# Performance work log

Measured on AMD Instinct MI355X. Metric: run time of the kernel, lower is better.

## Reference

```python
import jax, jax.numpy as jnp
import numpy as np

B, L, D = 2, 2048, 1024
H, DH = 16, 64
HIDDEN = 4096
DILATION, WINDOW, CAUSAL = 2, 512, True
EPS = 1e-5


def _ln(x, g, b):
    m = jnp.mean(x, axis=-1, keepdims=True)
    v = jnp.mean(jnp.square(x - m), axis=-1, keepdims=True)
    return (x - m) * jax.lax.rsqrt(v + EPS) * g + b


def setup_inputs() -> dict:
    key = jax.random.key(0)
    ks = jax.random.split(key, 8)
    s = 0.02
    return {
        "x": jax.random.normal(ks[0], (B, L, D), jnp.float32),
        "ln1_g": jnp.ones((D,), jnp.float32),
        "ln1_b": jnp.zeros((D,), jnp.float32),
        "w_qkv": jax.random.normal(ks[1], (3 * D, D), jnp.float32) * s,
        "b_qkv": jnp.zeros((3 * D,), jnp.float32),
        "w_o": jax.random.normal(ks[2], (D, D), jnp.float32) * s,
        "b_o": jnp.zeros((D,), jnp.float32),
        "ln2_g": jnp.ones((D,), jnp.float32),
        "ln2_b": jnp.zeros((D,), jnp.float32),
        "w_ff1": jax.random.normal(ks[3], (HIDDEN, D), jnp.float32) * s,
        "b_ff1": jnp.zeros((HIDDEN,), jnp.float32),
        "w_ff2": jax.random.normal(ks[4], (D, HIDDEN), jnp.float32) * s,
        "b_ff2": jnp.zeros((D,), jnp.float32),
    }


def reference(x, ln1_g, ln1_b, w_qkv, b_qkv, w_o, b_o, ln2_g, ln2_b, w_ff1, b_ff1, w_ff2, b_ff2):
    # pre-norm attention block with dilated/windowed/causal mask
    h = _ln(x, ln1_g, ln1_b)
    qkv = h @ w_qkv.T + b_qkv                      # [B, L, 3D]
    q, k, v = jnp.split(qkv, 3, axis=-1)
    q = q.reshape(B, L, H, DH)
    k = k.reshape(B, L, H, DH)
    v = v.reshape(B, L, H, DH)

    scale = 1.0 / jnp.sqrt(jnp.float32(DH))
    scores = jnp.einsum("bqhd,bkhd->bhqk", q, k) * scale  # [B, H, L, L]

    i = jnp.arange(L)[:, None]
    j = jnp.arange(L)[None, :]
    allowed = ((i - j) % DILATION == 0) & (jnp.abs(i - j) <= WINDOW)
    if CAUSAL:
        allowed = allowed & (j <= i)
    scores = jnp.where(allowed, scores, -jnp.inf)  # diagonal always allowed -> rows finite

    p = jax.nn.softmax(scores, axis=-1)
    attn = jnp.einsum("bhqk,bkhd->bqhd", p, v).reshape(B, L, D)

    out = x + attn @ w_o.T + b_o                   # residual 1 (dropout p=0)

    h2 = _ln(out, ln2_g, ln2_b)
    ff = jax.nn.gelu(h2 @ w_ff1.T + b_ff1, approximate=False) @ w_ff2.T + b_ff2
    return out + ff                                # residual 2
```

## Files before the change

kernel.cpp:

```cpp
#include <hip/hip_runtime.h>
#include <hip/hip_bf16.h>
#include <cmath>

#define Bsz 2
#define Lseq 2048
#define Dmod 1024
#define Hhead 16
#define DH 64
#define HID 4096
#define ROWS (Bsz * Lseq)
#define TD (3 * Dmod)

typedef __attribute__((ext_vector_type(8))) short bf16x8;
typedef __attribute__((ext_vector_type(4))) float f32x4;
typedef unsigned short ushort_t;

typedef const __attribute__((address_space(1))) void gv_t;
typedef __attribute__((address_space(3))) void lv_t;
#define GLDS16(GP, LP) __builtin_amdgcn_global_load_lds((gv_t*)(GP), (lv_t*)(LP), 16, 0, 0)

__device__ __forceinline__ float bf2f(short u)
{
    return __uint_as_float(((unsigned)(unsigned short)u) << 16);
}
__device__ __forceinline__ unsigned pack2(float a, float b)
{
    __hip_bfloat162 t;
    t.x = __float2bfloat16(a);
    t.y = __float2bfloat16(b);
    return *reinterpret_cast<unsigned*>(&t);
}
__device__ __forceinline__ float gelu_exact(float t)
{
    return 0.5f * t * (1.0f + erff(t * 0.70710678118654752f));
}

__device__ __forceinline__ void xcd_remap2(int cn, int cm, int& mblk, int& nblk)
{
    int nx = gridDim.x;
    int id = blockIdx.y * nx + blockIdx.x;
    int xcd = id & 7;
    int local = id >> 3;
    int gxn = nx / cn;
    int gx = xcd % gxn, gy = xcd / gxn;
    int ln = local % cn, lm = local / cn;
    nblk = gx * cn + ln;
    mblk = gy * cm + lm;
}

__global__ __launch_bounds__(256) void conv_q_ln1(const float* __restrict__ wsrc, ushort_t* __restrict__ wdst,
                                                  const float* __restrict__ x,
                                                  const float* __restrict__ g,
                                                  const float* __restrict__ bta,
                                                  ushort_t* __restrict__ lnout)
{
    int blk = blockIdx.x;
    int t = threadIdx.x;
    if (blk < 3072) {
        int i = blk * 256 + t;
        float4 v = reinterpret_cast<const float4*>(wsrc)[i];
        uint2 o;
        o.x = pack2(v.x, v.y);
        o.y = pack2(v.z, v.w);
        reinterpret_cast<uint2*>(wdst)[i] = o;
        return;
    }
    int row = blk - 3072;
    const float4* xr = reinterpret_cast<const float4*>(x) + (size_t)row * 256;
    float4 v = xr[t];
    float sum1 = v.x + v.y + v.z + v.w;
    float sum2 = v.x * v.x + v.y * v.y + v.z * v.z + v.w * v.w;
#pragma unroll
    for (int o = 32; o > 0; o >>= 1) {
        sum1 += __shfl_down(sum1, o);
        sum2 += __shfl_down(sum2, o);
    }
    __shared__ float sa[4], sb[4];
    int wv = t >> 6, ln = t & 63;
    if (ln == 0) { sa[wv] = sum1; sb[wv] = sum2; }
    __syncthreads();
    sum1 = sa[0] + sa[1] + sa[2] + sa[3];
    sum2 = sb[0] + sb[1] + sb[2] + sb[3];
    float mean = sum1 * (1.0f / 1024.0f);
    float var  = sum2 * (1.0f / 1024.0f) - mean * mean;
    float inv  = rsqrtf(var + 1e-5f);
    float4 gv = reinterpret_cast<const float4*>(g)[t];
    float4 bv = reinterpret_cast<const float4*>(bta)[t];
    uint2 o;
    o.x = pack2((v.x - mean) * inv * gv.x + bv.x, (v.y - mean) * inv * gv.y + bv.y);
    o.y = pack2((v.z - mean) * inv * gv.z + bv.z, (v.w - mean) * inv * gv.w + bv.w);
    reinterpret_cast<uint2*>(lnout)[(size_t)row * 256 + t] = o;
}

__global__ __launch_bounds__(256) void ln_kernel(const float* __restrict__ x,
                                                 const float* __restrict__ g,
                                                 const float* __restrict__ bta,
                                                 ushort_t* __restrict__ out)
{
    int row = blockIdx.x;
    int t = threadIdx.x;
    const float4* xr = reinterpret_cast<const float4*>(x) + (size_t)row * 256;
    float4 v = xr[t];
    float sum1 = v.x + v.y + v.z + v.w;
    float sum2 = v.x * v.x + v.y * v.y + v.z * v.z + v.w * v.w;
#pragma unroll
    for (int o = 32; o > 0; o >>= 1) {
        sum1 += __shfl_down(sum1, o);
        sum2 += __shfl_down(sum2, o);
    }
    __shared__ float sa[4], sb[4];
    int wv = t >> 6, ln = t & 63;
    if (ln == 0) { sa[wv] = sum1; sb[wv] = sum2; }
    __syncthreads();
    sum1 = sa[0] + sa[1] + sa[2] + sa[3];
    sum2 = sb[0] + sb[1] + sb[2] + sb[3];
    float mean = sum1 * (1.0f / 1024.0f);
    float var  = sum2 * (1.0f / 1024.0f) - mean * mean;
    float inv  = rsqrtf(var + 1e-5f);
    float4 gv = reinterpret_cast<const float4*>(g)[t];
    float4 bv = reinterpret_cast<const float4*>(bta)[t];
    uint2 o;
    o.x = pack2((v.x - mean) * inv * gv.x + bv.x, (v.y - mean) * inv * gv.y + bv.y);
    o.y = pack2((v.z - mean) * inv * gv.z + bv.z, (v.w - mean) * inv * gv.w + bv.w);
    reinterpret_cast<uint2*>(out)[(size_t)row * 256 + t] = o;
}

__device__ __forceinline__ void gemm_n64_body(const ushort_t* __restrict__ A,
                                              const ushort_t* __restrict__ W,
                                              const float* __restrict__ bias,
                                              const float* __restrict__ res,
                                              void* __restrict__ C,
                                              int M, int N, int K, int ldw,
                                              int act, int obf, int cn, int cm)
{
    __shared__ ushort_t As0[128 * 64];
    __shared__ ushort_t Bs0[64 * 64];
    __shared__ ushort_t As1[128 * 64];
    __shared__ ushort_t Bs1[64 * 64];

    int tid = threadIdx.x;
    int w = tid >> 6, lane = tid & 63;
    int mblk, nblk;
    xcd_remap2(cn, cm, mblk, nblk);
    int m0 = mblk * 128, n0 = nblk * 64;
    int wr = (w >> 1) * 64, wc = (w & 1) * 32;

    int srow = lane >> 3;
    int scol = (((lane & 7) ^ (lane >> 3)) & 7) * 8;
    const ushort_t* ga[4];
    const ushort_t* gb[2];
    int laofs[4], lbofs[2];
#pragma unroll
    for (int q = 0; q < 4; ++q) {
        ga[q] = A + (size_t)(m0 + w * 32 + q * 8 + srow) * K + scol;
        laofs[q] = (w * 32 + q * 8) * 64;
    }
#pragma unroll
    for (int q = 0; q < 2; ++q) {
        gb[q] = W + (size_t)(n0 + w * 16 + q * 8 + srow) * ldw + scol;
        lbofs[q] = (w * 16 + q * 8) * 64;
    }

    int fr = lane & 15;
    int fg = lane >> 4;
    int r0 = fg * 4;
    int cc = fr;

    f32x4 acc[4][2] = {};

    auto stage = [&](ushort_t* AS, ushort_t* BS, int k0) {
#pragma unroll
        for (int q = 0; q < 4; ++q) GLDS16(ga[q] + k0, AS + laofs[q]);
#pragma unroll
        for (int q = 0; q < 2; ++q) GLDS16(gb[q] + k0, BS + lbofs[q]);
    };
    auto compute = [&](const ushort_t* AS, const ushort_t* BS) {
#pragma unroll
        for (int kk = 0; kk < 2; ++kk) {
            bf16x8 af[4], bfr[2];
            int ca = ((kk * 4 + fg) ^ (fr & 7)) * 8;
#pragma unroll
            for (int i = 0; i < 4; ++i)
                af[i] = *reinterpret_cast<const bf16x8*>(&AS[(wr + i * 16 + fr) * 64 + ca]);
#pragma unroll
            for (int i = 0; i < 2; ++i)
                bfr[i] = *reinterpret_cast<const bf16x8*>(&BS[(wc + i * 16 + fr) * 64 + ca]);
#pragma unroll
            for (int mi = 0; mi < 4; ++mi)
#pragma unroll
                for (int ni = 0; ni < 2; ++ni)
                    acc[mi][ni] = __builtin_amdgcn_mfma_f32_16x16x32_bf16(
                        af[mi], bfr[ni], acc[mi][ni], 0, 0, 0);
        }
    };

    int nt = K >> 6;
    stage(As0, Bs0, 0);
    stage(As1, Bs1, 64);
    int t = 0;
    for (; t + 3 < nt; t += 2) {
        asm volatile("s_waitcnt vmcnt(6)" ::: "memory");
        __builtin_amdgcn_s_barrier();
        __builtin_amdgcn_sched_barrier(0);
        compute(As0, Bs0);
        __builtin_amdgcn_s_barrier();
        stage(As0, Bs0, (t + 2) * 64);

        asm volatile("s_waitcnt vmcnt(6)" ::: "memory");
        __builtin_amdgcn_s_barrier();
        __builtin_amdgcn_sched_barrier(0);
        compute(As1, Bs1);
        __builtin_amdgcn_s_barrier();
        stage(As1, Bs1, (t + 3) * 64);
    }
    asm volatile("s_waitcnt vmcnt(6)" ::: "memory");
    __builtin_amdgcn_s_barrier();
    __builtin_amdgcn_sched_barrier(0);
    compute(As0, Bs0);
    asm volatile("s_waitcnt vmcnt(0)" ::: "memory");
    __builtin_amdgcn_s_barrier();
    __builtin_amdgcn_sched_barrier(0);
    compute(As1, Bs1);

    float bv[2];
#pragma unroll
    for (int ni = 0; ni < 2; ++ni)
        bv[ni] = bias ? bias[n0 + wc + ni * 16 + cc] : 0.0f;

#pragma unroll
    for (int mi = 0; mi < 4; ++mi) {
#pragma unroll
        for (int r = 0; r < 4; ++r) {
            int row = m0 + wr + mi * 16 + r0 + r;
            const float* resrow = res ? res + (size_t)row * N : nullptr;
#pragma unroll
            for (int ni = 0; ni < 2; ++ni) {
                int col = n0 + wc + ni * 16 + cc;
                float v = acc[mi][ni][r] + bv[ni];
                if (act == 1) v = gelu_exact(v);
                if (resrow) v += resrow[col];
                if (obf) {
                    reinterpret_cast<ushort_t*>(C)[(size_t)row * N + col] =
                        (ushort_t)__bfloat16_as_ushort(__float2bfloat16(v));
                } else {
                    reinterpret_cast<float*>(C)[(size_t)row * N + col] = v;
                }
            }
        }
    }
}

__global__ __launch_bounds__(256) void gemm_a(const ushort_t* __restrict__ A,
                                              const ushort_t* __restrict__ W,
                                              const float* __restrict__ bias,
                                              const float* __restrict__ res,
                                              void* __restrict__ C,
                                              int M, int N, int K, int ldw,
                                              int act, int obf, int cn, int cm)
{
    gemm_n64_body(A, W, bias, res, C, M, N, K, ldw, act, obf, cn, cm);
}

__global__ __launch_bounds__(256) void gemm_b(const ushort_t* __restrict__ A,
                                              const ushort_t* __restrict__ W,
                                              const float* __restrict__ bias,
                                              const float* __restrict__ res,
                                              void* __restrict__ C,
                                              int M, int N, int K, int ldw,
                                              int act, int obf, int cn, int cm)
{
    gemm_n64_body(A, W, bias, res, C, M, N, K, ldw, act, obf, cn, cm);
}

__global__ __launch_bounds__(256) void attn_conv(const ushort_t* __restrict__ qkv,
                                                 ushort_t* __restrict__ out,
                                                 const float* __restrict__ w1, ushort_t* __restrict__ d1,
                                                 const float* __restrict__ w2, ushort_t* __restrict__ d2,
                                                 const float* __restrict__ w3, ushort_t* __restrict__ d3)
{
    __shared__ ushort_t Vt[64][328];
    __shared__ ushort_t Pw[4][16][40];

    int bid = blockIdx.x;
    int tid = threadIdx.x;

    if (bid >= 1024) {
        int blk = bid - 1024;
        const float* src;
        ushort_t* dst;
        int base;
        if (blk < 1024)      { src = w1; dst = d1; base = blk; }
        else if (blk < 5120) { src = w2; dst = d2; base = blk - 1024; }
        else                 { src = w3; dst = d3; base = blk - 5120; }
        int i = base * 256 + tid;
        float4 v = reinterpret_cast<const float4*>(src)[i];
        uint2 o;
        o.x = pack2(v.x, v.y);
        o.y = pack2(v.z, v.w);
        reinterpret_cast<uint2*>(dst)[i] = o;
        return;
    }

    int qt = bid & 15, h = (bid >> 4) & 15, p = (bid >> 8) & 1, b = bid >> 9;
    int qt0 = qt * 64;
    int kstart = qt0 - 256;

    const ushort_t* base = qkv + (size_t)b * Lseq * TD;

#pragma unroll
    for (int it = 0; it < 10; ++it) {
        int idx = it * 256 + tid;
        int ko = idx >> 3;
        int dg = idx & 7;
        int kk = kstart + ko;
        bf16x8 v = {};
        if (kk >= 0)
            v = *reinterpret_cast<const bf16x8*>(base + (size_t)(2 * kk + p) * TD + 2048 + h * 64 + dg * 8);
        int kos = ko ^ (dg << 3);
#pragma unroll
        for (int j = 0; j < 8; ++j)
            Vt[dg * 8 + j][kos] = (ushort_t)v[j];
    }

    int w = tid >> 6, lane = tid & 63;
    int fr = lane & 15, fg = lane >> 4;
    int qw = qt0 + w * 16;
    const ushort_t* qrow = base + (size_t)(2 * (qw + fr) + p) * TD + h * 64;
    bf16x8 qf0 = *reinterpret_cast<const bf16x8*>(qrow + fg * 8);
    bf16x8 qf1 = *reinterpret_cast<const bf16x8*>(qrow + 32 + fg * 8);

    __syncthreads();

    float m[4]    = {-1e30f, -1e30f, -1e30f, -1e30f};
    float lsum[4] = {};
    f32x4 o[4]    = {};
    const float scale = 0.125f;
    int qbase = qw + fg * 4;

    for (int t = 0; t < 10; ++t) {
        int kt0 = kstart + t * 32;
        int kk0 = kt0 + fr, kk1 = kk0 + 16;
        int kk0c = kk0 < 0 ? 0 : kk0;
        int kk1c = kk1 < 0 ? 0 : kk1;
        const ushort_t* kr0 = base + (size_t)(2 * kk0c + p) * TD + 1024 + h * 64;
        const ushort_t* kr1 = base + (size_t)(2 * kk1c + p) * TD + 1024 + h * 64;
        bf16x8 k00 = *reinterpret_cast<const bf16x8*>(kr0 + fg * 8);
        bf16x8 k01 = *reinterpret_cast<const bf16x8*>(kr0 + 32 + fg * 8);
        bf16x8 k10 = *reinterpret_cast<const bf16x8*>(kr1 + fg * 8);
        bf16x8 k11 = *reinterpret_cast<const bf16x8*>(kr1 + 32 + fg * 8);

        f32x4 s0 = {}, s1 = {};
        s0 = __builtin_amdgcn_mfma_f32_16x16x32_bf16(qf0, k00, s0, 0, 0, 0);
        s0 = __builtin_amdgcn_mfma_f32_16x16x32_bf16(qf1, k01, s0, 0, 0, 0);
        s1 = __builtin_amdgcn_mfma_f32_16x16x32_bf16(qf0, k10, s1, 0, 0, 0);
        s1 = __builtin_amdgcn_mfma_f32_16x16x32_bf16(qf1, k11, s1, 0, 0, 0);

        int c0 = kt0 + fr, c1 = c0 + 16;
        float v0[4], v1[4], tmax[4];
#pragma unroll
        for (int r = 0; r < 4; ++r) {
            int qq = qbase + r;
            bool a0 = (c0 >= 0) && (c0 <= qq) && (c0 >= qq - 256);
            bool a1 = (c1 >= 0) && (c1 <= qq) && (c1 >= qq - 256);
            v0[r] = a0 ? s0[r] * scale : -1e30f;
            v1[r] = a1 ? s1[r] * scale : -1e30f;
            tmax[r] = fmaxf(v0[r], v1[r]);
        }
#pragma unroll
        for (int off = 1; off < 16; off <<= 1) {
#pragma unroll
            for (int r = 0; r < 4; ++r)
                tmax[r] = fmaxf(tmax[r], __shfl_xor(tmax[r], off));
        }
#pragma unroll
        for (int r = 0; r < 4; ++r) {
            float mn = fmaxf(m[r], tmax[r]);
            float corr = __expf(m[r] - mn);
            m[r] = mn;
            float p0 = __expf(v0[r] - mn);
            float p1 = __expf(v1[r] - mn);
            lsum[r] = lsum[r] * corr + p0 + p1;
#pragma unroll
            for (int db = 0; db < 4; ++db)
                o[db][r] *= corr;
            Pw[w][fg * 4 + r][fr]      = (ushort_t)__bfloat16_as_ushort(__float2bfloat16(p0));
            Pw[w][fg * 4 + r][fr + 16] = (ushort_t)__bfloat16_as_ushort(__float2bfloat16(p1));
        }

        bf16x8 pf = *reinterpret_cast<const bf16x8*>(&Pw[w][fr][fg * 8]);
#pragma unroll
        for (int db = 0; db < 4; ++db) {
            int row = db * 16 + fr;
            int colc = (t * 32 + fg * 8) ^ ((row >> 3) << 3);
            bf16x8 vf = *reinterpret_cast<const bf16x8*>(&Vt[row][colc]);
            o[db] = __builtin_amdgcn_mfma_f32_16x16x32_bf16(pf, vf, o[db], 0, 0, 0);
        }
    }

#pragma unroll
    for (int off = 1; off < 16; off <<= 1) {
#pragma unroll
        for (int r = 0; r < 4; ++r)
            lsum[r] += __shfl_xor(lsum[r], off);
    }
    float inv[4];
#pragma unroll
    for (int r = 0; r < 4; ++r) inv[r] = 1.0f / lsum[r];

#pragma unroll
    for (int r = 0; r < 4; ++r) {
        size_t orow = ((size_t)b * Lseq + 2 * (qbase + r) + p) * Dmod + h * 64;
#pragma unroll
        for (int db = 0; db < 4; ++db)
            out[orow + db * 16 + fr] =
                (ushort_t)__bfloat16_as_ushort(__float2bfloat16(o[db][r] * inv[r]));
    }
}

extern "C" void kernel_launch(void* const* d_in, const int* in_sizes, int n_in,
                              void* d_out, int out_size, void* d_ws, size_t ws_size,
                              hipStream_t stream)
{
    const float* x     = (const float*)d_in[0];
    const float* ln1_g = (const float*)d_in[1];
    const float* ln1_b = (const float*)d_in[2];
    const float* w_qkv = (const float*)d_in[3];
    const float* b_qkv = (const float*)d_in[4];
    const float* w_o   = (const float*)d_in[5];
    const float* b_o   = (const float*)d_in[6];
    const float* ln2_g = (const float*)d_in[7];
    const float* ln2_b = (const float*)d_in[8];
    const float* w_ff1 = (const float*)d_in[9];
    const float* b_ff1 = (const float*)d_in[10];
    const float* w_ff2 = (const float*)d_in[11];
    const float* b_ff2 = (const float*)d_in[12];
    float* out = (float*)d_out;

    ushort_t* wq     = (ushort_t*)d_ws;
    ushort_t* wo     = wq  + (size_t)TD * Dmod;
    ushort_t* wf1    = wo  + (size_t)Dmod * Dmod;
    ushort_t* wf2    = wf1 + (size_t)HID * Dmod;
    ushort_t* bufFF  = wf2 + (size_t)Dmod * HID;
    ushort_t* bufH   = bufFF + (size_t)ROWS * HID;
    ushort_t* bufAtt = bufH + (size_t)ROWS * Dmod;

    conv_q_ln1<<<7168, 256, 0, stream>>>(w_qkv, wq, x, ln1_g, ln1_b, bufH);
    gemm_a<<<dim3(TD / 64, ROWS / 128), 256, 0, stream>>>(bufH, wq, b_qkv, nullptr,
                                                          bufFF, ROWS, TD, Dmod, Dmod, 0, 1,
                                                          12, 16);
    attn_conv<<<10240, 256, 0, stream>>>(bufFF, bufAtt, w_o, wo, w_ff1, wf1, w_ff2, wf2);
    gemm_b<<<dim3(Dmod / 64, ROWS / 128), 256, 0, stream>>>(bufAtt, wo, b_o, x,
                                                            out, ROWS, Dmod, Dmod, Dmod, 0, 0,
                                                            8, 8);
    ln_kernel<<<ROWS, 256, 0, stream>>>(out, ln2_g, ln2_b, bufH);
    gemm_a<<<dim3(HID / 64, ROWS / 128), 256, 0, stream>>>(bufH, wf1, b_ff1, nullptr,
                                                           bufFF, ROWS, HID, Dmod, Dmod, 1, 1,
                                                           16, 16);
    gemm_b<<<dim3(Dmod / 64, ROWS / 128), 256, 0, stream>>>(bufFF, wf2, b_ff2, out,
                                                            out, ROWS, Dmod, HID, HID, 0, 0,
                                                            8, 8);
}
```

Baseline: 215.9 us.

## Split-K the FF2 GEMM with atomic accumulation into the residual output

Replaces the final FF2 GEMM (M=4096, N=1024, K=4096, only 512 blocks) with a split-K kernel that uses two K halves and atomically adds partial sums into the output buffer, which already holds the residual. To keep the bias correct, b_ff2 is folded into the attention-projection epilogue, and the LN2 kernel subtracts it back before normalizing. The goal is more blocks to fill the GPU's CUs. The cost is fp32 atomic traffic and a summation order that is no longer deterministic.

```diff
diff --git a/kernel.cpp b/kernel.cpp
--- a/kernel.cpp
+++ b/kernel.cpp
@@ -95,12 +95,17 @@
 __global__ __launch_bounds__(256) void ln_kernel(const float* __restrict__ x,
                                                  const float* __restrict__ g,
                                                  const float* __restrict__ bta,
+                                                 const float* __restrict__ sub,
                                                  ushort_t* __restrict__ out)
 {
     int row = blockIdx.x;
     int t = threadIdx.x;
     const float4* xr = reinterpret_cast<const float4*>(x) + (size_t)row * 256;
     float4 v = xr[t];
+    if (sub) {
+        float4 s4 = reinterpret_cast<const float4*>(sub)[t];
+        v.x -= s4.x; v.y -= s4.y; v.z -= s4.z; v.w -= s4.w;
+    }
     float sum1 = v.x + v.y + v.z + v.w;
     float sum2 = v.x * v.x + v.y * v.y + v.z * v.z + v.w * v.w;
 #pragma unroll
@@ -128,6 +133,7 @@
 __device__ __forceinline__ void gemm_n64_body(const ushort_t* __restrict__ A,
                                               const ushort_t* __restrict__ W,
                                               const float* __restrict__ bias,
+                                              const float* __restrict__ bias2,
                                               const float* __restrict__ res,
                                               void* __restrict__ C,
                                               int M, int N, int K, int ldw,
@@ -224,8 +230,10 @@
 
     float bv[2];
 #pragma unroll
-    for (int ni = 0; ni < 2; ++ni)
+    for (int ni = 0; ni < 2; ++ni) {
         bv[ni] = bias ? bias[n0 + wc + ni * 16 + cc] : 0.0f;
+        if (bias2) bv[ni] += bias2[n0 + wc + ni * 16 + cc];
+    }
 
 #pragma unroll
     for (int mi = 0; mi < 4; ++mi) {
@@ -258,18 +266,129 @@
                                               int M, int N, int K, int ldw,
                                               int act, int obf, int cn, int cm)
 {
-    gemm_n64_body(A, W, bias, res, C, M, N, K, ldw, act, obf, cn, cm);
+    gemm_n64_body(A, W, bias, nullptr, res, C, M, N, K, ldw, act, obf, cn, cm);
 }
 
 __global__ __launch_bounds__(256) void gemm_b(const ushort_t* __restrict__ A,
                                               const ushort_t* __restrict__ W,
                                               const float* __restrict__ bias,
+                                              const float* __restrict__ bias2,
                                               const float* __restrict__ res,
                                               void* __restrict__ C,
                                               int M, int N, int K, int ldw,
                                               int act, int obf, int cn, int cm)
 {
-    gemm_n64_body(A, W, bias, res, C, M, N, K, ldw, act, obf, cn, cm);
+    gemm_n64_body(A, W, bias, bias2, res, C, M, N, K, ldw, act, obf, cn, cm);
+}
+
+__global__ __launch_bounds__(256) void gemm_sk(const ushort_t* __restrict__ A,
+                                               const ushort_t* __restrict__ W,
+                                               float* __restrict__ C,
+                                               int M, int N, int Kfull, int KH,
+                                               int cn, int cm)
+{
+    __shared__ ushort_t As0[128 * 64];
+    __shared__ ushort_t Bs0[64 * 64];
+    __shared__ ushort_t As1[128 * 64];
+    __shared__ ushort_t Bs1[64 * 64];
+
+    int tid = threadIdx.x;
+    int w = tid >> 6, lane = tid & 63;
+    int mblk, nblk;
+    xcd_remap2(cn, cm, mblk, nblk);
+    int m0 = mblk * 128, n0 = nblk * 64;
+    int wr = (w >> 1) * 64, wc = (w & 1) * 32;
+    int koff = blockIdx.z * KH;
+
+    int srow = lane >> 3;
+    int scol = (((lane & 7) ^ (lane >> 3)) & 7) * 8;
+    const ushort_t* ga[4];
+    const ushort_t* gb[2];
+    int laofs[4], lbofs[2];
+#pragma unroll
+    for (int q = 0; q < 4; ++q) {
+        ga[q] = A + (size_t)(m0 + w * 32 + q * 8 + srow) * Kfull + koff + scol;
+        laofs[q] = (w * 32 + q * 8) * 64;
+    }
+#pragma unroll
+    for (int q = 0; q < 2; ++q) {
+        gb[q] = W + (size_t)(n0 + w * 16 + q * 8 + srow) * Kfull + koff + scol;
+        lbofs[q] = (w * 16 + q * 8) * 64;
+    }
+
+    int fr = lane & 15;
+    int fg = lane >> 4;
+    int r0 = fg * 4;
+    int cc = fr;
+
+    f32x4 acc[4][2] = {};
+
+    auto stage = [&](ushort_t* AS, ushort_t* BS, int k0) {
+#pragma unroll
+        for (int q = 0; q < 4; ++q) GLDS16(ga[q] + k0, AS + laofs[q]);
+#pragma unroll
+        for (int q = 0; q < 2; ++q) GLDS16(gb[q] + k0, BS + lbofs[q]);
+    };
+    auto compute = [&](const ushort_t* AS, const ushort_t* BS) {
+#pragma unroll
+        for (int kk = 0; kk < 2; ++kk) {
+            bf16x8 af[4], bfr[2];
+            int ca = ((kk * 4 + fg) ^ (fr & 7)) * 8;
+#pragma unroll
+            for (int i = 0; i < 4; ++i)
+                af[i] = *reinterpret_cast<const bf16x8*>(&AS[(wr + i * 16 + fr) * 64 + ca]);
+#pragma unroll
+            for (int i = 0; i < 2; ++i)
+                bfr[i] = *reinterpret_cast<const bf16x8*>(&BS[(wc + i * 16 + fr) * 64 + ca]);
+#pragma unroll
+            for (int mi = 0; mi < 4; ++mi)
+#pragma unroll
+                for (int ni = 0; ni < 2; ++ni)
+                    acc[mi][ni] = __builtin_amdgcn_mfma_f32_16x16x32_bf16(
+                        af[mi], bfr[ni], acc[mi][ni], 0, 0, 0);
+        }
+    };
+
+    int nt = KH >> 6;
+    stage(As0, Bs0, 0);
+    stage(As1, Bs1, 64);
+    int t = 0;
+    for (; t + 3 < nt; t += 2) {
+        asm volatile("s_waitcnt vmcnt(6)" ::: "memory");
+        __builtin_amdgcn_s_barrier();
+        __builtin_amdgcn_sched_barrier(0);
+        compute(As0, Bs0);
+        __builtin_amdgcn_s_barrier();
+        stage(As0, Bs0, (t + 2) * 64);
+
+        asm volatile("s_waitcnt vmcnt(6)" ::: "memory");
+        __builtin_amdgcn_s_barrier();
+        __builtin_amdgcn_sched_barrier(0);
+        compute(As1, Bs1);
+        __builtin_amdgcn_s_barrier();
+        stage(As1, Bs1, (t + 3) * 64);
+    }
+    asm volatile("s_waitcnt vmcnt(6)" ::: "memory");
+    __builtin_amdgcn_s_barrier();
+    __builtin_amdgcn_sched_barrier(0);
+    compute(As0, Bs0);
+    asm volatile("s_waitcnt vmcnt(0)" ::: "memory");
+    __builtin_amdgcn_s_barrier();
+    __builtin_amdgcn_sched_barrier(0);
+    compute(As1, Bs1);
+
+#pragma unroll
+    for (int mi = 0; mi < 4; ++mi) {
+#pragma unroll
+        for (int r = 0; r < 4; ++r) {
+            int row = m0 + wr + mi * 16 + r0 + r;
+#pragma unroll
+            for (int ni = 0; ni < 2; ++ni) {
+                int col = n0 + wc + ni * 16 + cc;
+                atomicAdd(&C[(size_t)row * N + col], acc[mi][ni][r]);
+            }
+        }
+    }
 }
 
 __global__ __launch_bounds__(256) void attn_conv(const ushort_t* __restrict__ qkv,
@@ -449,14 +568,14 @@
                                                           bufFF, ROWS, TD, Dmod, Dmod, 0, 1,
                                                           12, 16);
     attn_conv<<<10240, 256, 0, stream>>>(bufFF, bufAtt, w_o, wo, w_ff1, wf1, w_ff2, wf2);
-    gemm_b<<<dim3(Dmod / 64, ROWS / 128), 256, 0, stream>>>(bufAtt, wo, b_o, x,
+    gemm_b<<<dim3(Dmod / 64, ROWS / 128), 256, 0, stream>>>(bufAtt, wo, b_o, b_ff2, x,
                                                             out, ROWS, Dmod, Dmod, Dmod, 0, 0,
                                                             8, 8);
-    ln_kernel<<<ROWS, 256, 0, stream>>>(out, ln2_g, ln2_b, bufH);
+    ln_kernel<<<ROWS, 256, 0, stream>>>(out, ln2_g, ln2_b, b_ff2, bufH);
     gemm_a<<<dim3(HID / 64, ROWS / 128), 256, 0, stream>>>(bufH, wf1, b_ff1, nullptr,
                                                            bufFF, ROWS, HID, Dmod, Dmod, 1, 1,
                                                            16, 16);
-    gemm_b<<<dim3(Dmod / 64, ROWS / 128), 256, 0, stream>>>(bufFF, wf2, b_ff2, out,
-                                                            out, ROWS, Dmod, HID, HID, 0, 0,
-                                                            8, 8);
-}
+    gemm_sk<<<dim3(Dmod / 64, ROWS / 128, 2), 256, 0, stream>>>(bufFF, wf2, out,
+                                                                ROWS, Dmod, HID, HID / 2,
+                                                                8, 8);
+}
```

Result: slower. 223.3 us (+3.4%).
